# Performance work log

Measured on AMD Instinct MI355X. Metric: run time of the kernel, lower is better.

## Reference

```python
import jax, jax.numpy as jnp
import numpy as np

NUM_CLASSES = 21
SHAPE = (64, 512, 512)


def setup_inputs() -> dict:
    key = jax.random.key(0)
    k1, k2 = jax.random.split(key)
    y_pred = jax.random.randint(k1, SHAPE, 0, NUM_CLASSES, dtype=jnp.int32)
    y_true = jax.random.randint(k2, SHAPE, 0, NUM_CLASSES, dtype=jnp.int32)
    return {"y_pred": y_pred, "y_true": y_true}


def reference(y_pred, y_true):
    # Faithful to the (buggy) source: target_inds is derived from y_pred,
    # so for each cls in 1..NUM_CLASSES-1: intersection == union == count(y_pred==cls).
    # iousSum += count>0 ? 1.0 : 0.0 (nan branch still adds 0/1 = 0).
    # Result = (#classes in [1, NUM_CLASSES) present in y_pred) / NUM_CLASSES.
    yp = y_pred.reshape(-1)
    counts = jnp.bincount(yp, length=NUM_CLASSES)  # single fused histogram, no per-class loop
    present = (counts[1:] > 0).astype(jnp.float32)  # classes 1..NUM_CLASSES-1
    return jnp.sum(present) / NUM_CLASSES
```

## Files before the change

kernel.cpp:

```cpp
#include <hip/hip_runtime.h>
#include <hip/hip_bf16.h>


#define NUM_CLASSES 21
#define SCAN_GRID 4096
#define SCAN_BLOCK 256

__global__ __launch_bounds__(SCAN_BLOCK) void miou_scan(
        const int* __restrict__ yp,
        unsigned int* __restrict__ block_masks,
        int n4) {
    const int4* __restrict__ yp4 = (const int4*)yp;
    const int idx = blockIdx.x * blockDim.x + threadIdx.x;
    const int stride = gridDim.x * blockDim.x;
    unsigned int m = 0u;

    if (n4 == 4 * stride) {
        int4 v0 = yp4[idx];
        int4 v1 = yp4[idx + stride];
        int4 v2 = yp4[idx + 2 * stride];
        int4 v3 = yp4[idx + 3 * stride];
        m = (1u << v0.x) | (1u << v0.y) | (1u << v0.z) | (1u << v0.w)
          | (1u << v1.x) | (1u << v1.y) | (1u << v1.z) | (1u << v1.w)
          | (1u << v2.x) | (1u << v2.y) | (1u << v2.z) | (1u << v2.w)
          | (1u << v3.x) | (1u << v3.y) | (1u << v3.z) | (1u << v3.w);
    } else {
        for (int i = idx; i < n4; i += stride) {
            int4 v = yp4[i];
            m |= (1u << v.x) | (1u << v.y) | (1u << v.z) | (1u << v.w);
        }
    }

    #pragma unroll
    for (int off = 32; off >= 1; off >>= 1) {
        m |= __shfl_xor(m, off, 64);
    }
    __shared__ unsigned int wmask[SCAN_BLOCK / 64];
    if ((threadIdx.x & 63) == 0) {
        wmask[threadIdx.x >> 6] = m;
    }
    __syncthreads();
    if (threadIdx.x == 0) {
        block_masks[blockIdx.x] = wmask[0] | wmask[1] | wmask[2] | wmask[3];
    }
}

__global__ __launch_bounds__(256) void miou_finalize(
        const unsigned int* __restrict__ block_masks,
        float* __restrict__ out,
        int nblocks) {
    unsigned int m = 0u;
    for (int i = threadIdx.x; i < nblocks; i += blockDim.x) {
        m |= block_masks[i];
    }
    #pragma unroll
    for (int off = 32; off >= 1; off >>= 1) {
        m |= __shfl_xor(m, off, 64);
    }
    __shared__ unsigned int wmask[4];
    if ((threadIdx.x & 63) == 0) {
        wmask[threadIdx.x >> 6] = m;
    }
    __syncthreads();
    if (threadIdx.x == 0) {
        unsigned int t = (wmask[0] | wmask[1] | wmask[2] | wmask[3]) & 0x001FFFFEu;
        out[0] = (float)__popc(t) / (float)NUM_CLASSES;
    }
}

extern "C" void kernel_launch(void* const* d_in, const int* in_sizes, int n_in,
                              void* d_out, int out_size, void* d_ws, size_t ws_size,
                              hipStream_t stream) {
    const int* y_pred = (const int*)d_in[0];
    float* out = (float*)d_out;
    unsigned int* block_masks = (unsigned int*)d_ws;

    int n = in_sizes[0];
    int n4 = n >> 2;

    miou_scan<<<SCAN_GRID, SCAN_BLOCK, 0, stream>>>(y_pred, block_masks, n4);
    miou_finalize<<<1, 256, 0, stream>>>(block_masks, out, SCAN_GRID);
}
```

Baseline: 133.2 us.

## Halve scan grid and give each wave a contiguous 8-vector chunk

Result: no change. 132.3 us (-0.6%).

```diff
diff --git a/kernel.cpp b/kernel.cpp
--- a/kernel.cpp
+++ b/kernel.cpp
@@ -3,28 +3,42 @@
 
 
 #define NUM_CLASSES 21
-#define SCAN_GRID 4096
+#define SCAN_GRID 2048
 #define SCAN_BLOCK 256
+#define WAVES_PER_BLOCK (SCAN_BLOCK / 64)
+#define VEC_PER_WAVE 512
 
 __global__ __launch_bounds__(SCAN_BLOCK) void miou_scan(
         const int* __restrict__ yp,
         unsigned int* __restrict__ block_masks,
         int n4) {
     const int4* __restrict__ yp4 = (const int4*)yp;
-    const int idx = blockIdx.x * blockDim.x + threadIdx.x;
-    const int stride = gridDim.x * blockDim.x;
+    const int lane = threadIdx.x & 63;
+    const int wave_in_block = threadIdx.x >> 6;
+    const int gwave = blockIdx.x * WAVES_PER_BLOCK + wave_in_block;
     unsigned int m = 0u;
 
-    if (n4 == 4 * stride) {
-        int4 v0 = yp4[idx];
-        int4 v1 = yp4[idx + stride];
-        int4 v2 = yp4[idx + 2 * stride];
-        int4 v3 = yp4[idx + 3 * stride];
-        m = (1u << v0.x) | (1u << v0.y) | (1u << v0.z) | (1u << v0.w)
-          | (1u << v1.x) | (1u << v1.y) | (1u << v1.z) | (1u << v1.w)
-          | (1u << v2.x) | (1u << v2.y) | (1u << v2.z) | (1u << v2.w)
-          | (1u << v3.x) | (1u << v3.y) | (1u << v3.z) | (1u << v3.w);
+    if (n4 == SCAN_GRID * WAVES_PER_BLOCK * VEC_PER_WAVE) {
+        const int base = gwave * VEC_PER_WAVE + lane;
+        int4 v0 = yp4[base + 0 * 64];
+        int4 v1 = yp4[base + 1 * 64];
+        int4 v2 = yp4[base + 2 * 64];
+        int4 v3 = yp4[base + 3 * 64];
+        int4 v4 = yp4[base + 4 * 64];
+        int4 v5 = yp4[base + 5 * 64];
+        int4 v6 = yp4[base + 6 * 64];
+        int4 v7 = yp4[base + 7 * 64];
+        m  = (1u << v0.x) | (1u << v0.y) | (1u << v0.z) | (1u << v0.w);
+        m |= (1u << v1.x) | (1u << v1.y) | (1u << v1.z) | (1u << v1.w);
+        m |= (1u << v2.x) | (1u << v2.y) | (1u << v2.z) | (1u << v2.w);
+        m |= (1u << v3.x) | (1u << v3.y) | (1u << v3.z) | (1u << v3.w);
+        m |= (1u << v4.x) | (1u << v4.y) | (1u << v4.z) | (1u << v4.w);
+        m |= (1u << v5.x) | (1u << v5.y) | (1u << v5.z) | (1u << v5.w);
+        m |= (1u << v6.x) | (1u << v6.y) | (1u << v6.z) | (1u << v6.w);
+        m |= (1u << v7.x) | (1u << v7.y) | (1u << v7.z) | (1u << v7.w);
     } else {
+        const int idx = blockIdx.x * blockDim.x + threadIdx.x;
+        const int stride = gridDim.x * blockDim.x;
         for (int i = idx; i < n4; i += stride) {
             int4 v = yp4[i];
             m |= (1u << v.x) | (1u << v.y) | (1u << v.z) | (1u << v.w);
@@ -35,9 +49,9 @@
     for (int off = 32; off >= 1; off >>= 1) {
         m |= __shfl_xor(m, off, 64);
     }
-    __shared__ unsigned int wmask[SCAN_BLOCK / 64];
-    if ((threadIdx.x & 63) == 0) {
-        wmask[threadIdx.x >> 6] = m;
+    __shared__ unsigned int wmask[WAVES_PER_BLOCK];
+    if (lane == 0) {
+        wmask[wave_in_block] = m;
     }
     __syncthreads();
     if (threadIdx.x == 0) {
```
